# Kernel tuning notes

Measured on AMD Instinct MI355X. Metric: run time of the kernel, lower is better.

Reference implementation:

```python
import jax, jax.numpy as jnp
import numpy as np
import math

B, L, D = 4, 4096, 1024
D_EMB, D_HID = 3, 16


def make_pos_emb(emb_dim, seq_len):
    # Complex exponential positional embeddings (non-trainable), shape (1, seq_len, emb_dim)
    t = np.linspace(0.0, 1.0, seq_len, dtype=np.float32)[None, :, None]
    bands = (emb_dim - 1) // 2
    t_res = np.linspace(0.0, seq_len - 1, seq_len, dtype=np.float32)[None, :, None]
    w = 2.0 * math.pi * t_res / seq_len
    f = np.linspace(0.0001, max(bands - 1, 0), bands, dtype=np.float32)[None, None]
    z = np.exp(-1j * (f * w).astype(np.complex64))
    z = np.concatenate([t, z.real.astype(np.float32), z.imag.astype(np.float32)], axis=-1)
    return jnp.asarray(z)


def setup_inputs() -> dict:
    key = jax.random.key(0)
    ks = jax.random.split(key, 8)
    u = jax.random.normal(ks[0], (B, L, D), dtype=jnp.float32)
    z = make_pos_emb(D_EMB, L)  # (1, L, D_EMB)
    # filter MLP: Linear(d_emb, d_hidden) -> ReLU -> Linear(d_hidden, d_model)
    s1 = 1.0 / math.sqrt(D_EMB)
    w1 = jax.random.uniform(ks[1], (D_HID, D_EMB), jnp.float32, -s1, s1)
    b1 = jax.random.uniform(ks[2], (D_HID,), jnp.float32, -s1, s1)
    s2 = 1.0 / math.sqrt(D_HID)
    w2 = jax.random.uniform(ks[3], (D, D_HID), jnp.float32, -s2, s2)
    b2 = jax.random.uniform(ks[4], (D,), jnp.float32, -s2, s2)
    # projection: Linear(d_model, d_model)
    sp = 1.0 / math.sqrt(D)
    pw = jax.random.uniform(ks[5], (D, D), jnp.float32, -sp, sp)
    pb = jax.random.uniform(ks[6], (D,), jnp.float32, -sp, sp)
    return {"u": u, "z": z, "w1": w1, "b1": b1, "w2": w2, "b2": b2, "pw": pw, "pb": pb}


def fft_conv(u_bdl, k_dl):
    # u_bdl: (B, D, L), k_dl: (1, D, L) or (D, L)
    seqlen = u_bdl.shape[-1]
    fft_size = 2 * seqlen
    k_f = jnp.fft.rfft(k_dl, n=fft_size) / fft_size
    u_f = jnp.fft.rfft(u_bdl, n=fft_size)
    y = jnp.fft.irfft(u_f * k_f, n=fft_size, norm="forward")[..., :seqlen]
    return y


def reference(u, z, w1, b1, w2, b2, pw, pb):
    seqlen = u.shape[1]
    pe = z[:, :seqlen]  # (1, L, D_EMB)
    h = jax.nn.relu(jnp.einsum("ble,he->blh", pe, w1) + b1)
    filt = jnp.einsum("blh,dh->bld", h, w2) + b2  # (1, L, D)
    filt = jnp.transpose(filt, (0, 2, 1))  # (1, D, L)
    u_conv = fft_conv(jnp.transpose(u, (0, 2, 1)), filt)  # (B, D, L)
    u_conv = jnp.transpose(u_conv, (0, 2, 1)).astype(u.dtype)  # (B, L, D)
    u_proj = jnp.einsum("bld,od->blo", u, pw) + pb
    return u_conv * u_proj + u
```

## Files before the change

kernel.cpp:

```cpp
#include <hip/hip_runtime.h>
#include <hip/hip_bf16.h>

#define SEQL 4096
#define DCH  1024
#define BATCH 4
#define NC   4096
#define KH   4097

typedef float2 cf;
__device__ __forceinline__ cf mkc(float x, float y){ return make_float2(x,y); }
__device__ __forceinline__ cf cadd(cf a, cf b){ return mkc(a.x+b.x, a.y+b.y); }
__device__ __forceinline__ cf csub(cf a, cf b){ return mkc(a.x-b.x, a.y-b.y); }
__device__ __forceinline__ cf cmul(cf a, cf b){ return mkc(a.x*b.x - a.y*b.y, a.x*b.y + a.y*b.x); }
__device__ __forceinline__ cf cconjf(cf a){ return mkc(a.x, -a.y); }
__device__ __forceinline__ cf addi(cf a, cf b){ return mkc(a.x - b.y, a.y + b.x); }
__device__ __forceinline__ cf subi(cf a, cf b){ return mkc(a.x + b.y, a.y - b.x); }
__device__ __forceinline__ int cpad(int i){ return i + (i >> 4); }
__device__ __forceinline__ int drev(int i){
    return ((i>>10)&3) | (((i>>8)&3)<<2) | (((i>>6)&3)<<4)
         | (((i>>4)&3)<<6) | (((i>>2)&3)<<8) | ((i&3)<<10);
}

__global__ __launch_bounds__(256) void twiddle_init(cf* __restrict__ tw4, cf* __restrict__ tw8){
    int i = blockIdx.x*256 + threadIdx.x;
    const double TWO_PI = 6.283185307179586476925286766559;
    double a4 = -TWO_PI * (double)i / 4096.0;
    double a8 = -TWO_PI * (double)i / 8192.0;
    tw4[i] = mkc((float)cos(a4), (float)sin(a4));
    tw8[i] = mkc((float)cos(a8), (float)sin(a8));
}

__device__ void fft_dif(cf* lds, const cf* __restrict__ tw){
    const int tid = threadIdx.x;
#pragma unroll
    for (int p = 0; p < 4; ++p) {
        const int lm = 10 - 2*p;
        const int m  = 1 << lm;
        const int step = 1024 >> lm;
#pragma unroll
        for (int it = 0; it < 4; ++it) {
            int j = tid + (it << 8);
            int k = j & (m-1);
            int g = j >> lm;
            int i0 = (g << (lm+2)) + k;
            cf x0 = lds[cpad(i0)];
            cf x1 = lds[cpad(i0+m)];
            cf x2 = lds[cpad(i0+2*m)];
            cf x3 = lds[cpad(i0+3*m)];
            cf b0 = cadd(x0,x2), b1 = csub(x0,x2);
            cf b2 = cadd(x1,x3), b3 = csub(x1,x3);
            cf u0 = cadd(b0,b2);
            cf u2 = csub(b0,b2);
            cf u1 = subi(b1,b3);
            cf u3 = addi(b1,b3);
            int t1 = k*step;
            lds[cpad(i0)]     = u0;
            lds[cpad(i0+m)]   = cmul(u1, tw[t1]);
            lds[cpad(i0+2*m)] = cmul(u2, tw[2*t1]);
            lds[cpad(i0+3*m)] = cmul(u3, tw[3*t1]);
        }
        __syncthreads();
    }
    {
        int base = 17*tid;
        cf v[16];
#pragma unroll
        for (int j=0;j<16;++j) v[j] = lds[base+j];
#pragma unroll
        for (int j=0;j<4;++j){
            cf x0=v[j], x1=v[j+4], x2=v[j+8], x3=v[j+12];
            cf b0=cadd(x0,x2), b1=csub(x0,x2), b2=cadd(x1,x3), b3=csub(x1,x3);
            cf u0=cadd(b0,b2), u2=csub(b0,b2), u1=subi(b1,b3), u3=addi(b1,b3);
            v[j]    = u0;
            v[j+4]  = cmul(u1, tw[256*j]);
            v[j+8]  = cmul(u2, tw[512*j]);
            v[j+12] = cmul(u3, tw[768*j]);
        }
#pragma unroll
        for (int c=0;c<4;++c){
            cf x0=v[4*c], x1=v[4*c+1], x2=v[4*c+2], x3=v[4*c+3];
            cf b0=cadd(x0,x2), b1=csub(x0,x2), b2=cadd(x1,x3), b3=csub(x1,x3);
            v[4*c]   = cadd(b0,b2);
            v[4*c+1] = subi(b1,b3);
            v[4*c+2] = csub(b0,b2);
            v[4*c+3] = addi(b1,b3);
        }
#pragma unroll
        for (int j=0;j<16;++j) lds[base+j] = v[j];
        __syncthreads();
    }
}

__device__ void fft_dit_inv(cf* lds, const cf* __restrict__ tw){
    const int tid = threadIdx.x;
    {
        int base = 17*tid;
        cf v[16];
#pragma unroll
        for (int j=0;j<16;++j) v[j] = lds[base+j];
#pragma unroll
        for (int c=0;c<4;++c){
            cf a0=v[4*c], a1=v[4*c+1], a2=v[4*c+2], a3=v[4*c+3];
            cf b0=cadd(a0,a2), b1=csub(a0,a2), b2=cadd(a1,a3), b3=csub(a1,a3);
            v[4*c]   = cadd(b0,b2);
            v[4*c+1] = addi(b1,b3);
            v[4*c+2] = csub(b0,b2);
            v[4*c+3] = subi(b1,b3);
        }
#pragma unroll
        for (int j=0;j<4;++j){
            cf a0=v[j];
            cf a1=cmul(v[j+4],  cconjf(tw[256*j]));
            cf a2=cmul(v[j+8],  cconjf(tw[512*j]));
            cf a3=cmul(v[j+12], cconjf(tw[768*j]));
            cf b0=cadd(a0,a2), b1=csub(a0,a2), b2=cadd(a1,a3), b3=csub(a1,a3);
            v[j]    = cadd(b0,b2);
            v[j+4]  = addi(b1,b3);
            v[j+8]  = csub(b0,b2);
            v[j+12] = subi(b1,b3);
        }
#pragma unroll
        for (int j=0;j<16;++j) lds[base+j] = v[j];
        __syncthreads();
    }
#pragma unroll
    for (int p = 0; p < 4; ++p) {
        const int lm = 4 + 2*p;
        const int m  = 1 << lm;
        const int step = 1024 >> lm;
#pragma unroll
        for (int it = 0; it < 4; ++it) {
            int j = tid + (it << 8);
            int k = j & (m-1);
            int g = j >> lm;
            int i0 = (g << (lm+2)) + k;
            int t1 = k*step;
            cf a0 = lds[cpad(i0)];
            cf a1 = cmul(lds[cpad(i0+m)],   cconjf(tw[t1]));
            cf a2 = cmul(lds[cpad(i0+2*m)], cconjf(tw[2*t1]));
            cf a3 = cmul(lds[cpad(i0+3*m)], cconjf(tw[3*t1]));
            cf b0=cadd(a0,a2), b1=csub(a0,a2), b2=cadd(a1,a3), b3=csub(a1,a3);
            lds[cpad(i0)]     = cadd(b0,b2);
            lds[cpad(i0+m)]   = addi(b1,b3);
            lds[cpad(i0+2*m)] = csub(b0,b2);
            lds[cpad(i0+3*m)] = subi(b1,b3);
        }
        __syncthreads();
    }
}

__global__ __launch_bounds__(256) void mlp_kernel(
        const float* __restrict__ z, const float* __restrict__ w1,
        const float* __restrict__ b1, float* __restrict__ h) {
    int l = blockIdx.x * blockDim.x + threadIdx.x;
    if (l >= SEQL) return;
    float pe0 = z[l * 3 + 0], pe1 = z[l * 3 + 1], pe2 = z[l * 3 + 2];
#pragma unroll
    for (int j = 0; j < 16; ++j) {
        float v = pe0 * w1[j * 3 + 0] + pe1 * w1[j * 3 + 1] + pe2 * w1[j * 3 + 2] + b1[j];
        h[l * 16 + j] = v > 0.f ? v : 0.f;
    }
}

__global__ __launch_bounds__(256) void transpose_kernel(
        const float* __restrict__ u, float* __restrict__ ut) {
    __shared__ float tile[32][33];
    int b = blockIdx.z;
    int l0 = blockIdx.x * 32;
    int d0 = blockIdx.y * 32;
    int tx = threadIdx.x, ty = threadIdx.y;
    const float* up = u + (size_t)b * SEQL * DCH;
#pragma unroll
    for (int i = 0; i < 32; i += 8)
        tile[ty + i][tx] = up[(size_t)(l0 + ty + i) * DCH + d0 + tx];
    __syncthreads();
    float* utp = ut + (size_t)b * DCH * SEQL;
#pragma unroll
    for (int i = 0; i < 32; i += 8)
        utp[(size_t)(d0 + ty + i) * SEQL + l0 + tx] = tile[tx][ty + i];
}

__global__ __launch_bounds__(256) void filt_fft_kernel(
        const float* __restrict__ h, const float* __restrict__ w2,
        const float* __restrict__ b2, const cf* __restrict__ tw4,
        const cf* __restrict__ tw8, cf* __restrict__ kf) {
    __shared__ cf lds[4352];
    int d = blockIdx.x;
    int tid = threadIdx.x;
    float w[16];
#pragma unroll
    for (int j = 0; j < 16; ++j) w[j] = w2[d * 16 + j];
    float bb = b2[d];
    for (int n = tid; n < 2048; n += 256) {
        const float* h0 = h + (size_t)(2*n) * 16;
        float f0 = bb, f1 = bb;
#pragma unroll
        for (int j = 0; j < 16; ++j) { f0 += h0[j] * w[j]; f1 += h0[16 + j] * w[j]; }
        lds[cpad(n)] = mkc(f0, f1);
    }
    for (int n = 2048 + tid; n < 4096; n += 256) lds[cpad(n)] = mkc(0.f, 0.f);
    __syncthreads();
    fft_dif(lds, tw4);
    const float s = 1.f / 8192.f;
    cf* Hrow = kf + (size_t)d * KH;
    for (int k = tid; k < 2048; k += 256) {
        if (k == 0) {
            cf c0 = lds[cpad(0)];
            Hrow[0]    = mkc((c0.x + c0.y) * s, 0.f);
            Hrow[4096] = mkc((c0.x - c0.y) * s, 0.f);
            cf c2 = lds[cpad(drev(2048))];
            Hrow[2048] = mkc(c2.x * s, -c2.y * s);
        } else {
            int kk = 4096 - k;
            cf ck  = lds[cpad(drev(k))];
            cf ckk = lds[cpad(drev(kk))];
            cf cc = cconjf(ckk);
            cf E  = mkc(0.5f*(ck.x+cc.x), 0.5f*(ck.y+cc.y));
            cf Dd = csub(ck, cc);
            cf O  = mkc(0.5f*Dd.y, -0.5f*Dd.x);
            cf wv = tw8[k];
            cf Xk  = cadd(E, cmul(wv, O));
            cf wp  = mkc(-wv.x, wv.y);
            cf Xkk = cadd(cconjf(E), cmul(wp, cconjf(O)));
            Hrow[k]  = mkc(Xk.x * s, Xk.y * s);
            Hrow[kk] = mkc(Xkk.x * s, Xkk.y * s);
        }
    }
}

__global__ __launch_bounds__(256) void conv_kernel(
        float* __restrict__ uty, const cf* __restrict__ tw4,
        const cf* __restrict__ tw8, const cf* __restrict__ kf) {
    __shared__ cf lds[4352];
    int row = blockIdx.x;
    int d = row & (DCH - 1);
    int tid = threadIdx.x;
    float* rp = uty + (size_t)row * SEQL;
    for (int n = tid; n < 2048; n += 256)
        lds[cpad(n)] = *(const float2*)&rp[2*n];
    for (int n = 2048 + tid; n < 4096; n += 256) lds[cpad(n)] = mkc(0.f, 0.f);
    __syncthreads();
    fft_dif(lds, tw4);
    const cf* Hrow = kf + (size_t)d * KH;
    for (int k = tid; k < 2048; k += 256) {
        if (k == 0) {
            cf c0 = lds[cpad(0)];
            float X0 = c0.x + c0.y, X4 = c0.x - c0.y;
            cf H0 = Hrow[0], H4 = Hrow[4096];
            cf Y0 = mkc(X0 * H0.x, X0 * H0.y);
            cf Y4 = mkc(X4 * H4.x, X4 * H4.y);
            cf S  = cadd(Y0, Y4), Dd = csub(Y0, Y4);
            lds[cpad(0)] = addi(S, Dd);
            int s2 = cpad(drev(2048));
            cf c2 = lds[s2];
            cf Y2 = cmul(cconjf(c2), Hrow[2048]);
            lds[s2] = mkc(2.f * Y2.x, -2.f * Y2.y);
        } else {
            int kk = 4096 - k;
            int sk = cpad(drev(k)), skk = cpad(drev(kk));
            cf ck = lds[sk], ckk = lds[skk];
            cf cc = cconjf(ckk);
            cf E  = mkc(0.5f*(ck.x+cc.x), 0.5f*(ck.y+cc.y));
            cf Dd = csub(ck, cc);
            cf O  = mkc(0.5f*Dd.y, -0.5f*Dd.x);
            cf wv = tw8[k];
            cf Xk  = cadd(E, cmul(wv, O));
            cf wp  = mkc(-wv.x, wv.y);
            cf Xkk = cadd(cconjf(E), cmul(wp, cconjf(O)));
            cf Yk  = cmul(Xk,  Hrow[k]);
            cf Ykk = cmul(Xkk, Hrow[kk]);
            cf cy = cconjf(Ykk);
            cf S  = cadd(Yk, cy), D2 = csub(Yk, cy);
            cf Zk = addi(S, cmul(cconjf(wv), D2));
            cf cy2 = cconjf(Yk);
            cf S2  = cadd(Ykk, cy2), D3 = csub(Ykk, cy2);
            cf Zkk = subi(S2, cmul(wv, D3));
            lds[sk] = Zk; lds[skk] = Zkk;
        }
    }
    __syncthreads();
    fft_dit_inv(lds, tw4);
    for (int n = tid; n < 2048; n += 256) {
        cf v = lds[cpad(n)];
        *(float2*)&rp[2*n] = v;
    }
}

__device__ __forceinline__ unsigned pack2bf(float a, float b){
    unsigned r;
    asm("v_cvt_pk_bf16_f32 %0, %1, %2" : "=v"(r) : "v"(a), "v"(b));
    return r;
}

typedef __attribute__((ext_vector_type(8))) short short8;
typedef __attribute__((ext_vector_type(4))) float f32x4;

__global__ __launch_bounds__(256, 3) void gemm_mfma_kernel(
        const float* __restrict__ u, const float* __restrict__ pw,
        const float* __restrict__ pb, const float* __restrict__ y,
        float* __restrict__ out) {
    __shared__ char lds_raw[34816];
    float (*ysc)[132] = (float(*)[132])lds_raw;

    const int tid  = threadIdx.x;
    const int lane = tid & 63;
    const int wid  = tid >> 6;
    const int wr   = wid >> 1;
    const int wc   = wid & 1;
    const int m0   = blockIdx.x * 128;
    const int n0   = blockIdx.y * 128;

    f32x4 acc[4][4] = {};
    float4 ra[4], rb[4];

    int s_row[4], s_f4[4];
#pragma unroll
    for (int j = 0; j < 4; ++j) {
        int idx = j * 256 + tid;
        s_row[j] = idx >> 3;
        s_f4[j]  = idx & 7;
    }

#define LOADT(kt)                                                                     \
    {                                                                                 \
        _Pragma("unroll")                                                             \
        for (int j = 0; j < 4; ++j) {                                                 \
            ra[j] = *(const float4*)&u [(size_t)(m0 + s_row[j]) * DCH + (kt) + s_f4[j] * 4]; \
            rb[j] = *(const float4*)&pw[(size_t)(n0 + s_row[j]) * DCH + (kt) + s_f4[j] * 4]; \
        }                                                                             \
    }
#define WRITET(base)                                                                  \
    {                                                                                 \
        _Pragma("unroll")                                                             \
        for (int j = 0; j < 4; ++j) {                                                 \
            int off = (base) + ((s_row[j] * 64 + s_f4[j] * 8) ^ ((s_row[j] & 3) << 4)); \
            uint2 pa, pbv2;                                                           \
            pa.x   = pack2bf(ra[j].x, ra[j].y);  pa.y   = pack2bf(ra[j].z, ra[j].w);  \
            pbv2.x = pack2bf(rb[j].x, rb[j].y);  pbv2.y = pack2bf(rb[j].z, rb[j].w);  \
            *(uint2*)(lds_raw + off)        = pa;                                     \
            *(uint2*)(lds_raw + off + 8192) = pbv2;                                   \
        }                                                                             \
    }

    LOADT(0);
    WRITET(0);
    LOADT(32);
    __syncthreads();

    for (int t = 0; t < 32; ++t) {
        const int cur = (t & 1) << 14;
        short8 af[4], bf[4];
#pragma unroll
        for (int f = 0; f < 4; ++f) {
            int rowA = wr * 64 + f * 16 + (lane & 15);
            int rowB = wc * 64 + f * 16 + (lane & 15);
            int offA = cur + ((rowA * 64 + ((lane >> 4) * 16)) ^ ((rowA & 3) << 4));
            int offB = cur + 8192 + ((rowB * 64 + ((lane >> 4) * 16)) ^ ((rowB & 3) << 4));
            af[f] = *(short8*)(lds_raw + offA);
            bf[f] = *(short8*)(lds_raw + offB);
        }
        if (t < 31) WRITET(cur ^ 16384);
        if (t < 30) LOADT((t + 2) * 32);
#pragma unroll
        for (int mf = 0; mf < 4; ++mf)
#pragma unroll
            for (int nf = 0; nf < 4; ++nf)
                acc[mf][nf] = __builtin_amdgcn_mfma_f32_16x16x32_bf16(
                    af[mf], bf[nf], acc[mf][nf], 0, 0, 0);
        __syncthreads();
    }

    const int b  = m0 >> 12;
    const int l0 = m0 & (SEQL - 1);
    float pbv[4];
#pragma unroll
    for (int nf = 0; nf < 4; ++nf)
        pbv[nf] = pb[n0 + wc * 64 + nf * 16 + (lane & 15)];

    for (int c = 0; c < 2; ++c) {
        __syncthreads();
#pragma unroll
        for (int j = 0; j < 8; ++j) {
            int idx = j * 256 + tid;
            int dn  = idx >> 4;
            int lf4 = idx & 15;
            float4 vy = *(const float4*)&y[(((size_t)(b * DCH + n0 + dn)) << 12) + l0 + c * 64 + lf4 * 4];
            ysc[lf4 * 4 + 0][dn] = vy.x;
            ysc[lf4 * 4 + 1][dn] = vy.y;
            ysc[lf4 * 4 + 2][dn] = vy.z;
            ysc[lf4 * 4 + 3][dn] = vy.w;
        }
        __syncthreads();
        if (wr == c) {
#pragma unroll
            for (int mf = 0; mf < 4; ++mf)
#pragma unroll
                for (int i = 0; i < 4; ++i) {
                    int lrow = mf * 16 + (lane >> 4) * 4 + i;
                    int m = m0 + c * 64 + lrow;
#pragma unroll
                    for (int nf = 0; nf < 4; ++nf) {
                        int nl = wc * 64 + nf * 16 + (lane & 15);
                        int n = n0 + nl;
                        float proj = acc[mf][nf][i] + pbv[nf];
                        out[(size_t)m * DCH + n] = ysc[lrow][nl] * proj + u[(size_t)m * DCH + n];
                    }
                }
        }
    }
#undef LOADT
#undef WRITET
}

extern "C" void kernel_launch(void* const* d_in, const int* in_sizes, int n_in,
                              void* d_out, int out_size, void* d_ws, size_t ws_size,
                              hipStream_t stream) {
    const float* u  = (const float*)d_in[0];
    const float* z  = (const float*)d_in[1];
    const float* w1 = (const float*)d_in[2];
    const float* b1 = (const float*)d_in[3];
    const float* w2 = (const float*)d_in[4];
    const float* b2 = (const float*)d_in[5];
    const float* pw = (const float*)d_in[6];
    const float* pb = (const float*)d_in[7];
    float* out = (float*)d_out;

    float* h   = (float*)d_ws;
    float* uty = (float*)((char*)d_ws + 262144);
    cf* kf  = (cf*)d_out;
    cf* tw4 = (cf*)((char*)d_out + (40u << 20));
    cf* tw8 = tw4 + 4096;

    twiddle_init<<<dim3(16), dim3(256), 0, stream>>>(tw4, tw8);
    mlp_kernel<<<dim3(16), dim3(256), 0, stream>>>(z, w1, b1, h);
    transpose_kernel<<<dim3(SEQL / 32, DCH / 32, BATCH), dim3(32, 8), 0, stream>>>(u, uty);
    filt_fft_kernel<<<dim3(DCH), dim3(256), 0, stream>>>(h, w2, b2, tw4, tw8, kf);
    conv_kernel<<<dim3(BATCH * DCH), dim3(256), 0, stream>>>(uty, tw4, tw8, kf);
    gemm_mfma_kernel<<<dim3(128, 8), dim3(256), 0, stream>>>(u, pw, pb, uty, out);
}
```

Measured before the change: 280.5 us.

## Rewrite 4096-point FFTs as three register radix-16 passes with XOR-swizzled LDS

```diff
diff --git a/kernel.cpp b/kernel.cpp
--- a/kernel.cpp
+++ b/kernel.cpp
@@ -4,7 +4,6 @@
 #define SEQL 4096
 #define DCH  1024
 #define BATCH 4
-#define NC   4096
 #define KH   4097
 
 typedef float2 cf;
@@ -15,10 +14,73 @@
 __device__ __forceinline__ cf cconjf(cf a){ return mkc(a.x, -a.y); }
 __device__ __forceinline__ cf addi(cf a, cf b){ return mkc(a.x - b.y, a.y + b.x); }
 __device__ __forceinline__ cf subi(cf a, cf b){ return mkc(a.x + b.y, a.y - b.x); }
-__device__ __forceinline__ int cpad(int i){ return i + (i >> 4); }
-__device__ __forceinline__ int drev(int i){
-    return ((i>>10)&3) | (((i>>8)&3)<<2) | (((i>>6)&3)<<4)
-         | (((i>>4)&3)<<6) | (((i>>2)&3)<<8) | ((i&3)<<10);
+
+__device__ __forceinline__ int phi(int c){ return c ^ (((c>>4)&7)<<1); }
+__device__ __forceinline__ int drev16(int i){ return ((i&15)<<8) | (i&0xF0) | (i>>8); }
+
+__device__ __forceinline__ void radix16_fwd(cf* v){
+    cf t[16];
+#pragma unroll
+    for (int a = 0; a < 4; ++a) {
+        cf x0 = v[a], x1 = v[a+4], x2 = v[a+8], x3 = v[a+12];
+        cf b0 = cadd(x0,x2), b1 = csub(x0,x2);
+        cf b2 = cadd(x1,x3), b3 = csub(x1,x3);
+        t[a*4+0] = cadd(b0,b2);
+        t[a*4+1] = subi(b1,b3);
+        t[a*4+2] = csub(b0,b2);
+        t[a*4+3] = addi(b1,b3);
+    }
+    t[5]  = cmul(t[5],  mkc( 0.92387953f, -0.38268343f));
+    t[6]  = cmul(t[6],  mkc( 0.70710678f, -0.70710678f));
+    t[7]  = cmul(t[7],  mkc( 0.38268343f, -0.92387953f));
+    t[9]  = cmul(t[9],  mkc( 0.70710678f, -0.70710678f));
+    t[10] = mkc(t[10].y, -t[10].x);
+    t[11] = cmul(t[11], mkc(-0.70710678f, -0.70710678f));
+    t[13] = cmul(t[13], mkc( 0.38268343f, -0.92387953f));
+    t[14] = cmul(t[14], mkc(-0.70710678f, -0.70710678f));
+    t[15] = cmul(t[15], mkc(-0.92387953f,  0.38268343f));
+#pragma unroll
+    for (int r = 0; r < 4; ++r) {
+        cf x0 = t[r], x1 = t[4+r], x2 = t[8+r], x3 = t[12+r];
+        cf b0 = cadd(x0,x2), b1 = csub(x0,x2);
+        cf b2 = cadd(x1,x3), b3 = csub(x1,x3);
+        v[0+r]  = cadd(b0,b2);
+        v[4+r]  = subi(b1,b3);
+        v[8+r]  = csub(b0,b2);
+        v[12+r] = addi(b1,b3);
+    }
+}
+__device__ __forceinline__ void radix16_inv(cf* v){
+    cf t[16];
+#pragma unroll
+    for (int a = 0; a < 4; ++a) {
+        cf x0 = v[a], x1 = v[a+4], x2 = v[a+8], x3 = v[a+12];
+        cf b0 = cadd(x0,x2), b1 = csub(x0,x2);
+        cf b2 = cadd(x1,x3), b3 = csub(x1,x3);
+        t[a*4+0] = cadd(b0,b2);
+        t[a*4+1] = addi(b1,b3);
+        t[a*4+2] = csub(b0,b2);
+        t[a*4+3] = subi(b1,b3);
+    }
+    t[5]  = cmul(t[5],  mkc( 0.92387953f,  0.38268343f));
+    t[6]  = cmul(t[6],  mkc( 0.70710678f,  0.70710678f));
+    t[7]  = cmul(t[7],  mkc( 0.38268343f,  0.92387953f));
+    t[9]  = cmul(t[9],  mkc( 0.70710678f,  0.70710678f));
+    t[10] = mkc(-t[10].y, t[10].x);
+    t[11] = cmul(t[11], mkc(-0.70710678f,  0.70710678f));
+    t[13] = cmul(t[13], mkc( 0.38268343f,  0.92387953f));
+    t[14] = cmul(t[14], mkc(-0.70710678f,  0.70710678f));
+    t[15] = cmul(t[15], mkc(-0.92387953f, -0.38268343f));
+#pragma unroll
+    for (int r = 0; r < 4; ++r) {
+        cf x0 = t[r], x1 = t[4+r], x2 = t[8+r], x3 = t[12+r];
+        cf b0 = cadd(x0,x2), b1 = csub(x0,x2);
+        cf b2 = cadd(x1,x3), b3 = csub(x1,x3);
+        v[0+r]  = cadd(b0,b2);
+        v[4+r]  = addi(b1,b3);
+        v[8+r]  = csub(b0,b2);
+        v[12+r] = subi(b1,b3);
+    }
 }
 
 __global__ __launch_bounds__(256) void twiddle_init(cf* __restrict__ tw4, cf* __restrict__ tw8){
@@ -28,125 +90,6 @@
     double a8 = -TWO_PI * (double)i / 8192.0;
     tw4[i] = mkc((float)cos(a4), (float)sin(a4));
     tw8[i] = mkc((float)cos(a8), (float)sin(a8));
-}
-
-__device__ void fft_dif(cf* lds, const cf* __restrict__ tw){
-    const int tid = threadIdx.x;
-#pragma unroll
-    for (int p = 0; p < 4; ++p) {
-        const int lm = 10 - 2*p;
-        const int m  = 1 << lm;
-        const int step = 1024 >> lm;
-#pragma unroll
-        for (int it = 0; it < 4; ++it) {
-            int j = tid + (it << 8);
-            int k = j & (m-1);
-            int g = j >> lm;
-            int i0 = (g << (lm+2)) + k;
-            cf x0 = lds[cpad(i0)];
-            cf x1 = lds[cpad(i0+m)];
-            cf x2 = lds[cpad(i0+2*m)];
-            cf x3 = lds[cpad(i0+3*m)];
-            cf b0 = cadd(x0,x2), b1 = csub(x0,x2);
-            cf b2 = cadd(x1,x3), b3 = csub(x1,x3);
-            cf u0 = cadd(b0,b2);
-            cf u2 = csub(b0,b2);
-            cf u1 = subi(b1,b3);
-            cf u3 = addi(b1,b3);
-            int t1 = k*step;
-            lds[cpad(i0)]     = u0;
-            lds[cpad(i0+m)]   = cmul(u1, tw[t1]);
-            lds[cpad(i0+2*m)] = cmul(u2, tw[2*t1]);
-            lds[cpad(i0+3*m)] = cmul(u3, tw[3*t1]);
-        }
-        __syncthreads();
-    }
-    {
-        int base = 17*tid;
-        cf v[16];
-#pragma unroll
-        for (int j=0;j<16;++j) v[j] = lds[base+j];
-#pragma unroll
-        for (int j=0;j<4;++j){
-            cf x0=v[j], x1=v[j+4], x2=v[j+8], x3=v[j+12];
-            cf b0=cadd(x0,x2), b1=csub(x0,x2), b2=cadd(x1,x3), b3=csub(x1,x3);
-            cf u0=cadd(b0,b2), u2=csub(b0,b2), u1=subi(b1,b3), u3=addi(b1,b3);
-            v[j]    = u0;
-            v[j+4]  = cmul(u1, tw[256*j]);
-            v[j+8]  = cmul(u2, tw[512*j]);
-            v[j+12] = cmul(u3, tw[768*j]);
-        }
-#pragma unroll
-        for (int c=0;c<4;++c){
-            cf x0=v[4*c], x1=v[4*c+1], x2=v[4*c+2], x3=v[4*c+3];
-            cf b0=cadd(x0,x2), b1=csub(x0,x2), b2=cadd(x1,x3), b3=csub(x1,x3);
-            v[4*c]   = cadd(b0,b2);
-            v[4*c+1] = subi(b1,b3);
-            v[4*c+2] = csub(b0,b2);
-            v[4*c+3] = addi(b1,b3);
-        }
-#pragma unroll
-        for (int j=0;j<16;++j) lds[base+j] = v[j];
-        __syncthreads();
-    }
-}
-
-__device__ void fft_dit_inv(cf* lds, const cf* __restrict__ tw){
-    const int tid = threadIdx.x;
-    {
-        int base = 17*tid;
-        cf v[16];
-#pragma unroll
-        for (int j=0;j<16;++j) v[j] = lds[base+j];
-#pragma unroll
-        for (int c=0;c<4;++c){
-            cf a0=v[4*c], a1=v[4*c+1], a2=v[4*c+2], a3=v[4*c+3];
-            cf b0=cadd(a0,a2), b1=csub(a0,a2), b2=cadd(a1,a3), b3=csub(a1,a3);
-            v[4*c]   = cadd(b0,b2);
-            v[4*c+1] = addi(b1,b3);
-            v[4*c+2] = csub(b0,b2);
-            v[4*c+3] = subi(b1,b3);
-        }
-#pragma unroll
-        for (int j=0;j<4;++j){
-            cf a0=v[j];
-            cf a1=cmul(v[j+4],  cconjf(tw[256*j]));
-            cf a2=cmul(v[j+8],  cconjf(tw[512*j]));
-            cf a3=cmul(v[j+12], cconjf(tw[768*j]));
-            cf b0=cadd(a0,a2), b1=csub(a0,a2), b2=cadd(a1,a3), b3=csub(a1,a3);
-            v[j]    = cadd(b0,b2);
-            v[j+4]  = addi(b1,b3);
-            v[j+8]  = csub(b0,b2);
-            v[j+12] = subi(b1,b3);
-        }
-#pragma unroll
-        for (int j=0;j<16;++j) lds[base+j] = v[j];
-        __syncthreads();
-    }
-#pragma unroll
-    for (int p = 0; p < 4; ++p) {
-        const int lm = 4 + 2*p;
-        const int m  = 1 << lm;
-        const int step = 1024 >> lm;
-#pragma unroll
-        for (int it = 0; it < 4; ++it) {
-            int j = tid + (it << 8);
-            int k = j & (m-1);
-            int g = j >> lm;
-            int i0 = (g << (lm+2)) + k;
-            int t1 = k*step;
-            cf a0 = lds[cpad(i0)];
-            cf a1 = cmul(lds[cpad(i0+m)],   cconjf(tw[t1]));
-            cf a2 = cmul(lds[cpad(i0+2*m)], cconjf(tw[2*t1]));
-            cf a3 = cmul(lds[cpad(i0+3*m)], cconjf(tw[3*t1]));
-            cf b0=cadd(a0,a2), b1=csub(a0,a2), b2=cadd(a1,a3), b3=csub(a1,a3);
-            lds[cpad(i0)]     = cadd(b0,b2);
-            lds[cpad(i0+m)]   = addi(b1,b3);
-            lds[cpad(i0+2*m)] = csub(b0,b2);
-            lds[cpad(i0+3*m)] = subi(b1,b3);
-        }
-        __syncthreads();
-    }
 }
 
 __global__ __launch_bounds__(256) void mlp_kernel(
@@ -180,47 +123,83 @@
         utp[(size_t)(d0 + ty + i) * SEQL + l0 + tx] = tile[tx][ty + i];
 }
 
-__global__ __launch_bounds__(256) void filt_fft_kernel(
+__global__ __launch_bounds__(256, 4) void filt_fft_kernel(
         const float* __restrict__ h, const float* __restrict__ w2,
         const float* __restrict__ b2, const cf* __restrict__ tw4,
         const cf* __restrict__ tw8, cf* __restrict__ kf) {
-    __shared__ cf lds[4352];
-    int d = blockIdx.x;
-    int tid = threadIdx.x;
-    float w[16];
-#pragma unroll
-    for (int j = 0; j < 16; ++j) w[j] = w2[d * 16 + j];
-    float bb = b2[d];
-    for (int n = tid; n < 2048; n += 256) {
-        const float* h0 = h + (size_t)(2*n) * 16;
+    __shared__ cf lds[4096];
+    const int d = blockIdx.x;
+    const int tid = threadIdx.x;
+    float wv[16];
+#pragma unroll
+    for (int j = 0; j < 16; ++j) wv[j] = w2[d * 16 + j];
+    const float bb = b2[d];
+    cf v[16];
+#pragma unroll
+    for (int j = 0; j < 8; ++j) {
+        int n = 2 * (tid + 256 * j);
+        const float* h0 = h + (size_t)n * 16;
         float f0 = bb, f1 = bb;
 #pragma unroll
-        for (int j = 0; j < 16; ++j) { f0 += h0[j] * w[j]; f1 += h0[16 + j] * w[j]; }
-        lds[cpad(n)] = mkc(f0, f1);
-    }
-    for (int n = 2048 + tid; n < 4096; n += 256) lds[cpad(n)] = mkc(0.f, 0.f);
-    __syncthreads();
-    fft_dif(lds, tw4);
+        for (int i = 0; i < 16; ++i) { f0 += h0[i] * wv[i]; f1 += h0[16 + i] * wv[i]; }
+        v[j] = mkc(f0, f1);
+    }
+#pragma unroll
+    for (int j = 8; j < 16; ++j) v[j] = mkc(0.f, 0.f);
+    radix16_fwd(v);
+    {
+        const int b0 = tid ^ (((tid >> 4) & 7) << 1);
+#pragma unroll
+        for (int j = 1; j < 16; ++j) v[j] = cmul(v[j], tw4[tid * j]);
+#pragma unroll
+        for (int j = 0; j < 16; ++j) lds[b0 + 256 * j] = v[j];
+    }
+    __syncthreads();
+    {
+        const int base = ((tid >> 4) << 8) | (tid & 15);
+        const int k = tid & 15;
+#pragma unroll
+        for (int j = 0; j < 16; ++j) v[j] = lds[(base + 16 * j) ^ ((j & 7) << 1)];
+        radix16_fwd(v);
+#pragma unroll
+        for (int j = 1; j < 16; ++j) v[j] = cmul(v[j], tw4[16 * k * j]);
+#pragma unroll
+        for (int j = 0; j < 16; ++j) lds[(base + 16 * j) ^ ((j & 7) << 1)] = v[j];
+    }
+    __syncthreads();
+    {
+        const int b0 = tid << 4;
+        const int xr = (tid & 7) << 1;
+#pragma unroll
+        for (int j = 0; j < 16; ++j) v[j] = lds[b0 + (j ^ xr)];
+        radix16_fwd(v);
+#pragma unroll
+        for (int j = 0; j < 16; ++j) lds[b0 + (j ^ xr)] = v[j];
+    }
+    __syncthreads();
     const float s = 1.f / 8192.f;
     cf* Hrow = kf + (size_t)d * KH;
-    for (int k = tid; k < 2048; k += 256) {
+    const int l = tid & 63, w = tid >> 6;
+#pragma unroll
+    for (int it = 0; it < 8; ++it) {
+        int k = ((l & 7) << 8) + ((l >> 3) << 5) + (it << 2) + w;
         if (k == 0) {
-            cf c0 = lds[cpad(0)];
+            cf c0 = lds[0];
             Hrow[0]    = mkc((c0.x + c0.y) * s, 0.f);
             Hrow[4096] = mkc((c0.x - c0.y) * s, 0.f);
-            cf c2 = lds[cpad(drev(2048))];
+            cf c2 = lds[8];
             Hrow[2048] = mkc(c2.x * s, -c2.y * s);
         } else {
             int kk = 4096 - k;
-            cf ck  = lds[cpad(drev(k))];
-            cf ckk = lds[cpad(drev(kk))];
+            cf ck  = lds[phi(drev16(k))];
+            cf ckk = lds[phi(drev16(kk))];
             cf cc = cconjf(ckk);
             cf E  = mkc(0.5f*(ck.x+cc.x), 0.5f*(ck.y+cc.y));
             cf Dd = csub(ck, cc);
             cf O  = mkc(0.5f*Dd.y, -0.5f*Dd.x);
-            cf wv = tw8[k];
-            cf Xk  = cadd(E, cmul(wv, O));
-            cf wp  = mkc(-wv.x, wv.y);
+            cf wvv = tw8[k];
+            cf Xk  = cadd(E, cmul(wvv, O));
+            cf wp  = mkc(-wvv.x, wvv.y);
             cf Xkk = cadd(cconjf(E), cmul(wp, cconjf(O)));
             Hrow[k]  = mkc(Xk.x * s, Xk.y * s);
             Hrow[kk] = mkc(Xkk.x * s, Xkk.y * s);
@@ -228,61 +207,123 @@
     }
 }
 
-__global__ __launch_bounds__(256) void conv_kernel(
+__global__ __launch_bounds__(256, 4) void conv_kernel(
         float* __restrict__ uty, const cf* __restrict__ tw4,
         const cf* __restrict__ tw8, const cf* __restrict__ kf) {
-    __shared__ cf lds[4352];
-    int row = blockIdx.x;
-    int d = row & (DCH - 1);
-    int tid = threadIdx.x;
+    __shared__ cf lds[4096];
+    const int row = blockIdx.x;
+    const int d = row & (DCH - 1);
+    const int tid = threadIdx.x;
     float* rp = uty + (size_t)row * SEQL;
-    for (int n = tid; n < 2048; n += 256)
-        lds[cpad(n)] = *(const float2*)&rp[2*n];
-    for (int n = 2048 + tid; n < 4096; n += 256) lds[cpad(n)] = mkc(0.f, 0.f);
-    __syncthreads();
-    fft_dif(lds, tw4);
+    cf v[16];
+#pragma unroll
+    for (int j = 0; j < 8; ++j) v[j] = *(const cf*)&rp[2 * (tid + 256 * j)];
+#pragma unroll
+    for (int j = 8; j < 16; ++j) v[j] = mkc(0.f, 0.f);
+    radix16_fwd(v);
+    {
+        const int b0 = tid ^ (((tid >> 4) & 7) << 1);
+#pragma unroll
+        for (int j = 1; j < 16; ++j) v[j] = cmul(v[j], tw4[tid * j]);
+#pragma unroll
+        for (int j = 0; j < 16; ++j) lds[b0 + 256 * j] = v[j];
+    }
+    __syncthreads();
+    {
+        const int base = ((tid >> 4) << 8) | (tid & 15);
+        const int k = tid & 15;
+#pragma unroll
+        for (int j = 0; j < 16; ++j) v[j] = lds[(base + 16 * j) ^ ((j & 7) << 1)];
+        radix16_fwd(v);
+#pragma unroll
+        for (int j = 1; j < 16; ++j) v[j] = cmul(v[j], tw4[16 * k * j]);
+#pragma unroll
+        for (int j = 0; j < 16; ++j) lds[(base + 16 * j) ^ ((j & 7) << 1)] = v[j];
+    }
+    __syncthreads();
+    {
+        const int b0 = tid << 4;
+        const int xr = (tid & 7) << 1;
+#pragma unroll
+        for (int j = 0; j < 16; ++j) v[j] = lds[b0 + (j ^ xr)];
+        radix16_fwd(v);
+#pragma unroll
+        for (int j = 0; j < 16; ++j) lds[b0 + (j ^ xr)] = v[j];
+    }
+    __syncthreads();
     const cf* Hrow = kf + (size_t)d * KH;
-    for (int k = tid; k < 2048; k += 256) {
-        if (k == 0) {
-            cf c0 = lds[cpad(0)];
-            float X0 = c0.x + c0.y, X4 = c0.x - c0.y;
-            cf H0 = Hrow[0], H4 = Hrow[4096];
-            cf Y0 = mkc(X0 * H0.x, X0 * H0.y);
-            cf Y4 = mkc(X4 * H4.x, X4 * H4.y);
-            cf S  = cadd(Y0, Y4), Dd = csub(Y0, Y4);
-            lds[cpad(0)] = addi(S, Dd);
-            int s2 = cpad(drev(2048));
-            cf c2 = lds[s2];
-            cf Y2 = cmul(cconjf(c2), Hrow[2048]);
-            lds[s2] = mkc(2.f * Y2.x, -2.f * Y2.y);
-        } else {
-            int kk = 4096 - k;
-            int sk = cpad(drev(k)), skk = cpad(drev(kk));
-            cf ck = lds[sk], ckk = lds[skk];
-            cf cc = cconjf(ckk);
-            cf E  = mkc(0.5f*(ck.x+cc.x), 0.5f*(ck.y+cc.y));
-            cf Dd = csub(ck, cc);
-            cf O  = mkc(0.5f*Dd.y, -0.5f*Dd.x);
-            cf wv = tw8[k];
-            cf Xk  = cadd(E, cmul(wv, O));
-            cf wp  = mkc(-wv.x, wv.y);
-            cf Xkk = cadd(cconjf(E), cmul(wp, cconjf(O)));
-            cf Yk  = cmul(Xk,  Hrow[k]);
-            cf Ykk = cmul(Xkk, Hrow[kk]);
-            cf cy = cconjf(Ykk);
-            cf S  = cadd(Yk, cy), D2 = csub(Yk, cy);
-            cf Zk = addi(S, cmul(cconjf(wv), D2));
-            cf cy2 = cconjf(Yk);
-            cf S2  = cadd(Ykk, cy2), D3 = csub(Ykk, cy2);
-            cf Zkk = subi(S2, cmul(wv, D3));
-            lds[sk] = Zk; lds[skk] = Zkk;
+    {
+        const int l = tid & 63, w = tid >> 6;
+#pragma unroll
+        for (int it = 0; it < 8; ++it) {
+            int k = ((l & 7) << 8) + ((l >> 3) << 5) + (it << 2) + w;
+            if (k == 0) {
+                cf c0 = lds[0];
+                float X0 = c0.x + c0.y, X4 = c0.x - c0.y;
+                cf H0 = Hrow[0], H4 = Hrow[4096];
+                cf Y0 = mkc(X0 * H0.x, X0 * H0.y);
+                cf Y4 = mkc(X4 * H4.x, X4 * H4.y);
+                cf S  = cadd(Y0, Y4), Dd = csub(Y0, Y4);
+                lds[0] = addi(S, Dd);
+                cf c2 = lds[8];
+                cf Y2 = cmul(cconjf(c2), Hrow[2048]);
+                lds[8] = mkc(2.f * Y2.x, -2.f * Y2.y);
+            } else {
+                int kk = 4096 - k;
+                int sk = phi(drev16(k)), skk = phi(drev16(kk));
+                cf ck = lds[sk], ckk = lds[skk];
+                cf cc = cconjf(ckk);
+                cf E  = mkc(0.5f*(ck.x+cc.x), 0.5f*(ck.y+cc.y));
+                cf Dd = csub(ck, cc);
+                cf O  = mkc(0.5f*Dd.y, -0.5f*Dd.x);
+                cf wv = tw8[k];
+                cf Xk  = cadd(E, cmul(wv, O));
+                cf wp  = mkc(-wv.x, wv.y);
+                cf Xkk = cadd(cconjf(E), cmul(wp, cconjf(O)));
+                cf Yk  = cmul(Xk,  Hrow[k]);
+                cf Ykk = cmul(Xkk, Hrow[kk]);
+                cf cy = cconjf(Ykk);
+                cf S  = cadd(Yk, cy), D2 = csub(Yk, cy);
+                cf Zk = addi(S, cmul(cconjf(wv), D2));
+                cf cy2 = cconjf(Yk);
+                cf S2  = cadd(Ykk, cy2), D3 = csub(Ykk, cy2);
+                cf Zkk = subi(S2, cmul(wv, D3));
+                lds[sk] = Zk; lds[skk] = Zkk;
+            }
         }
     }
     __syncthreads();
-    fft_dit_inv(lds, tw4);
-    for (int n = tid; n < 2048; n += 256) {
-        cf v = lds[cpad(n)];
-        *(float2*)&rp[2*n] = v;
+    {
+        const int b0 = tid << 4;
+        const int xr = (tid & 7) << 1;
+#pragma unroll
+        for (int j = 0; j < 16; ++j) v[j] = lds[b0 + (j ^ xr)];
+        radix16_inv(v);
+#pragma unroll
+        for (int j = 0; j < 16; ++j) lds[b0 + (j ^ xr)] = v[j];
+    }
+    __syncthreads();
+    {
+        const int base = ((tid >> 4) << 8) | (tid & 15);
+        const int k = tid & 15;
+#pragma unroll
+        for (int j = 0; j < 16; ++j) v[j] = lds[(base + 16 * j) ^ ((j & 7) << 1)];
+#pragma unroll
+        for (int j = 1; j < 16; ++j) v[j] = cmul(v[j], cconjf(tw4[16 * k * j]));
+        radix16_inv(v);
+#pragma unroll
+        for (int j = 0; j < 16; ++j) lds[(base + 16 * j) ^ ((j & 7) << 1)] = v[j];
+    }
+    __syncthreads();
+    {
+        const int b0 = tid ^ (((tid >> 4) & 7) << 1);
+#pragma unroll
+        for (int j = 0; j < 16; ++j) v[j] = lds[b0 + 256 * j];
+#pragma unroll
+        for (int j = 1; j < 16; ++j) v[j] = cmul(v[j], cconjf(tw4[tid * j]));
+        radix16_inv(v);
+#pragma unroll
+        for (int j = 0; j < 8; ++j) *(cf*)&rp[2 * (tid + 256 * j)] = v[j];
     }
 }
 
```

New measurement: 346.2 us. 1.23x slower.
